# Kernel optimization log

Hardware: AMD Instinct MI355X
Metric: run time of the kernel (lower is better)

The kernel has to match this reference:

```python
import jax, jax.numpy as jnp
import numpy as np

B, CIN, COUT, H, W = 8, 64, 64, 128, 128


def conv2d(x, w, b):
    # NCHW x OIHW -> NCHW, stride 1, SAME padding (kernel 3, pad 1)
    y = jax.lax.conv_general_dilated(
        x, w, window_strides=(1, 1), padding='SAME',
        dimension_numbers=('NCHW', 'OIHW', 'NCHW'))
    return y + b[None, :, None, None]


def bilinear_sample(img, py, px):
    # img: [B, C, H, W]; py, px: [B, K, H, W] float sample coords (y, x)
    # Zero padding outside the image (torchvision DeformConv2d semantics).
    Bn, C, Hn, Wn = img.shape
    y0 = jnp.floor(py)
    x0 = jnp.floor(px)
    wy = py - y0  # [B, K, H, W]
    wx = px - x0
    flat = img.reshape(Bn, C, Hn * Wn)

    def corner(yi, xi):
        valid = (yi >= 0) & (yi < Hn) & (xi >= 0) & (xi < Wn)
        yc = jnp.clip(yi, 0, Hn - 1).astype(jnp.int32)
        xc = jnp.clip(xi, 0, Wn - 1).astype(jnp.int32)
        idx = (yc * Wn + xc).reshape(Bn, -1)  # [B, K*H*W]
        g = jax.vmap(lambda f, i: f[:, i])(flat, idx)  # [B, C, K*H*W]
        g = g.reshape(Bn, C, *py.shape[1:])  # [B, C, K, H, W]
        return g * valid[:, None].astype(img.dtype)

    g00 = corner(y0, x0)
    g01 = corner(y0, x0 + 1)
    g10 = corner(y0 + 1, x0)
    g11 = corner(y0 + 1, x0 + 1)
    wy_ = wy[:, None]  # [B, 1, K, H, W]
    wx_ = wx[:, None]
    return (1 - wy_) * ((1 - wx_) * g00 + wx_ * g01) + wy_ * ((1 - wx_) * g10 + wx_ * g11)


def setup_inputs() -> dict:
    key = jax.random.key(0)
    ks = jax.random.split(key, 4)
    x = jax.random.normal(ks[0], (B, CIN, H, W), dtype=jnp.float32)
    # offset conv: in_channels -> 18 (= 2 * 3 * 3), kernel 3, pad 1
    offset_w = jax.random.normal(ks[1], (18, CIN, 3, 3), dtype=jnp.float32) * 0.01
    offset_b = jnp.zeros((18,), dtype=jnp.float32)
    deform_w = jax.random.normal(ks[2], (COUT, CIN, 3, 3), dtype=jnp.float32) * (1.0 / np.sqrt(CIN * 9))
    deform_b = jnp.zeros((COUT,), dtype=jnp.float32)
    return {'x': x, 'offset_w': offset_w, 'offset_b': offset_b,
            'deform_w': deform_w, 'deform_b': deform_b}


def reference(x, offset_w, offset_b, deform_w, deform_b):
    Bn, C, Hn, Wn = x.shape
    # 1) offset conv
    off = conv2d(x, offset_w, offset_b)  # [B, 18, H, W]
    off = off.reshape(Bn, 9, 2, Hn, Wn)  # per kernel position k: (dy, dx)
    dy = off[:, :, 0]  # [B, 9, H, W]
    dx = off[:, :, 1]
    # 2) sampling positions: p0 + p_k + offset (kernel 3x3, pad 1 -> p_k in {-1,0,1})
    k = jnp.arange(9)
    ki = (k // 3 - 1).astype(jnp.float32)[None, :, None, None]
    kj = (k % 3 - 1).astype(jnp.float32)[None, :, None, None]
    py = jnp.arange(Hn, dtype=jnp.float32)[None, None, :, None] + ki + dy
    px = jnp.arange(Wn, dtype=jnp.float32)[None, None, None, :] + kj + dx
    sampled = bilinear_sample(x, py, px)  # [B, C, 9, H, W]
    # 3) conv accumulation over (C, k)
    w = deform_w.reshape(deform_w.shape[0], C, 9)  # [O, C, 9]
    out = jnp.einsum('bckhw,ock->bohw', sampled, w) + deform_b[None, :, None, None]
    return jax.nn.relu(out)
```

## Files before the change

### kernel.cpp

```cpp
#include <hip/hip_runtime.h>
#include <hip/hip_bf16.h>

#define H_ 128
#define W_ 128
#define B_ 8
#define CIN_ 64
#define COUT_ 64

typedef __attribute__((ext_vector_type(8))) short bf16x8;
typedef __attribute__((ext_vector_type(4))) float f32x4;

static __device__ __forceinline__ unsigned short f2bf(float f) {
  union { float f; unsigned int u; } a; a.f = f;
  unsigned int u = a.u;
  return (unsigned short)((u + 0x7fffu + ((u >> 16) & 1u)) >> 16);
}
static __device__ __forceinline__ float bf2f(unsigned short h) {
  union { unsigned int u; float f; } a; a.u = ((unsigned int)h) << 16; return a.f;
}

__global__ __launch_bounds__(256) void prep_w(const float* __restrict__ dw,
    const float* __restrict__ ow, unsigned short* __restrict__ dwt,
    unsigned short* __restrict__ owt) {
  int id = blockIdx.x * 256 + threadIdx.x;
  if (id < 36864) {
    int c = id & 63, o = (id >> 6) & 63, k = id >> 12;
    dwt[id] = f2bf(dw[(o * 64 + c) * 9 + k]);
  } else if (id < 36864 + 18432) {
    int j = id - 36864;
    int c = j & 63, om = (j >> 6) & 31, t = j >> 11;
    owt[j] = f2bf(om < 18 ? ow[(om * 64 + c) * 9 + t] : 0.f);
  }
}


__device__ __forceinline__ void corner8(const float* __restrict__ x,
    const unsigned short* __restrict__ ldsx, int b, int iy, int ix,
    int oy, int ox, int c8, float g[8]) {
  int ly = iy - oy, lx = ix - ox;
  if ((unsigned)ly < 15u && (unsigned)lx < 16u) {
    int pt = (ly << 4) | lx;
    bf16x8 q = *(const bf16x8*)&ldsx[(pt << 6) | ((c8 ^ (pt & 7)) << 3)];
#pragma unroll
    for (int ci = 0; ci < 8; ++ci) g[ci] = bf2f((unsigned short)q[ci]);
  } else if ((unsigned)iy < (unsigned)H_ && (unsigned)ix < (unsigned)W_) {
#pragma unroll
    for (int ci = 0; ci < 8; ++ci)
      g[ci] = x[((b * CIN_ + (c8 << 3) + ci) * H_ + iy) * W_ + ix];
  } else {
#pragma unroll
    for (int ci = 0; ci < 8; ++ci) g[ci] = 0.f;
  }
}

__global__ __launch_bounds__(256) void deform_main(const float* __restrict__ x,
    const unsigned short* __restrict__ owt, const float* __restrict__ ob,
    const unsigned short* __restrict__ dwt, const float* __restrict__ db,
    float* __restrict__ out) {
  __shared__ unsigned short ldsx[240 * 64];
  __shared__ unsigned short ldsS[64 * 64];
  __shared__ float offs_lds[64][18];
  __shared__ int   p_iy[576], p_ix[576];
  __shared__ float p_wy[576], p_wx[576];

  const int tid = threadIdx.x;
  const int blk = blockIdx.x;
  const int b = blk >> 8;
  const int ty = ((blk >> 4) & 15) << 3;
  const int tx = (blk & 15) << 3;
  const int oy = ty - 3, ox = tx - 4;
  const int lane = tid & 63;
  const int wv = tid >> 6;
  const int o_m = (wv << 4) + (lane & 15);
  const int kgrp = lane >> 4;

  for (int i = 0; i < 15; ++i) {
    int it = tid + (i << 8);
    int c = it / 60;
    int r = it - c * 60;
    int lyy = r >> 2;
    int xq = r & 3;
    int gy = oy + lyy;
    int gx0 = ox + (xq << 2);
    float4 v = make_float4(0.f, 0.f, 0.f, 0.f);
    if ((unsigned)gy < (unsigned)H_ && (unsigned)gx0 < (unsigned)W_)
      v = *(const float4*)&x[((b * CIN_ + c) * H_ + gy) * W_ + gx0];
    int c8 = c >> 3, c0 = c & 7;
    const float vv[4] = {v.x, v.y, v.z, v.w};
#pragma unroll
    for (int q = 0; q < 4; ++q) {
      int pt = (lyy << 4) | ((xq << 2) + q);
      ldsx[(pt << 6) | ((c8 ^ (pt & 7)) << 3) | c0] = f2bf(vv[q]);
    }
  }
  __syncthreads();

  {
    f32x4 aoff0 = (f32x4){0.f, 0.f, 0.f, 0.f};
    f32x4 aoff1 = (f32x4){0.f, 0.f, 0.f, 0.f};
    const int pixw = (wv << 4) | (lane & 15);
#pragma unroll
    for (int t = 0; t < 9; ++t) {
      const int ti = t / 3 - 1, tj = t % 3 - 1;
      const int ly = (pixw >> 3) + ti + 3;
      const int lx = (pixw & 7) + tj + 4;
      const int pt = (ly << 4) | lx;
#pragma unroll
      for (int hf = 0; hf < 2; ++hf) {
        const int c8 = (hf << 2) | kgrp;
        bf16x8 bfr = *(const bf16x8*)&ldsx[(pt << 6) | ((c8 ^ (pt & 7)) << 3)];
        bf16x8 a0 = *(const bf16x8*)&owt[(((t << 5) | (lane & 15)) << 6) | (c8 << 3)];
        bf16x8 a1 = *(const bf16x8*)&owt[(((t << 5) | 16 | (lane & 15)) << 6) | (c8 << 3)];
        aoff0 = __builtin_amdgcn_mfma_f32_16x16x32_bf16(a0, bfr, aoff0, 0, 0, 0);
        aoff1 = __builtin_amdgcn_mfma_f32_16x16x32_bf16(a1, bfr, aoff1, 0, 0, 0);
      }
    }
#pragma unroll
    for (int j = 0; j < 4; ++j) {
      int o = (kgrp << 2) + j;
      offs_lds[pixw][o] = aoff0[j] + ob[o];
      int o1 = 16 + o;
      if (o1 < 18) offs_lds[pixw][o1] = aoff1[j] + ob[o1];
    }
  }
  __syncthreads();

  for (int u = tid; u < 576; u += 256) {
    int pix = u & 63, k = u >> 6;
    int yy = ty + (pix >> 3), xx = tx + (pix & 7);
    float dy = offs_lds[pix][2 * k];
    float dx = offs_lds[pix][2 * k + 1];
    float py = (float)(yy + k / 3 - 1) + dy;
    float px = (float)(xx + k % 3 - 1) + dx;
    float fy = floorf(py), fx = floorf(px);
    p_iy[u] = (int)fy; p_ix[u] = (int)fx;
    p_wy[u] = py - fy; p_wx[u] = px - fx;
  }
  __syncthreads();

  f32x4 acc[4];
#pragma unroll
  for (int nt = 0; nt < 4; ++nt) acc[nt] = (f32x4){0.f, 0.f, 0.f, 0.f};

#pragma unroll
  for (int k = 0; k < 9; ++k) {
    bf16x8 af0 = *(const bf16x8*)&dwt[(k << 12) + (o_m << 6) + (kgrp << 3)];
    bf16x8 af1 = *(const bf16x8*)&dwt[(k << 12) + (o_m << 6) + 32 + (kgrp << 3)];

#pragma unroll
    for (int i = 0; i < 2; ++i) {
      int u = tid + (i << 8);
      int pix = u >> 3, c8 = u & 7;
      int pd = (k << 6) | pix;
      int iy = p_iy[pd], ix = p_ix[pd];
      float wy = p_wy[pd], wx = p_wx[pd];
      float w00 = (1.f - wy) * (1.f - wx), w01 = (1.f - wy) * wx;
      float w10 = wy * (1.f - wx),         w11 = wy * wx;
      float g00[8], g01[8], g10[8], g11[8];
      corner8(x, ldsx, b, iy,     ix,     oy, ox, c8, g00);
      corner8(x, ldsx, b, iy,     ix + 1, oy, ox, c8, g01);
      corner8(x, ldsx, b, iy + 1, ix,     oy, ox, c8, g10);
      corner8(x, ldsx, b, iy + 1, ix + 1, oy, ox, c8, g11);
      bf16x8 sv;
#pragma unroll
      for (int ci = 0; ci < 8; ++ci) {
        float v = g00[ci] * w00 + g01[ci] * w01 + g10[ci] * w10 + g11[ci] * w11;
        sv[ci] = (short)f2bf(v);
      }
      *(bf16x8*)&ldsS[(pix << 6) | ((c8 ^ (pix & 7)) << 3)] = sv;
    }
    __syncthreads();

#pragma unroll
    for (int hf = 0; hf < 2; ++hf) {
#pragma unroll
      for (int nt = 0; nt < 4; ++nt) {
        int pix = (nt << 4) | (lane & 15);
        int c8 = (hf << 2) | kgrp;
        bf16x8 bf = *(const bf16x8*)&ldsS[(pix << 6) | ((c8 ^ (pix & 7)) << 3)];
        acc[nt] = __builtin_amdgcn_mfma_f32_16x16x32_bf16(hf ? af1 : af0, bf, acc[nt], 0, 0, 0);
      }
    }
    __syncthreads();
  }

#pragma unroll
  for (int nt = 0; nt < 4; ++nt) {
    int pix = (nt << 4) | (lane & 15);
    int gy = ty + (pix >> 3), gx = tx + (pix & 7);
#pragma unroll
    for (int j = 0; j < 4; ++j) {
      int o = (wv << 4) + (kgrp << 2) + j;
      float v = acc[nt][j] + db[o];
      out[((b * COUT_ + o) * H_ + gy) * W_ + gx] = v > 0.f ? v : 0.f;
    }
  }
}

extern "C" void kernel_launch(void* const* d_in, const int* in_sizes, int n_in,
                              void* d_out, int out_size, void* d_ws, size_t ws_size,
                              hipStream_t stream) {
  const float* x  = (const float*)d_in[0];
  const float* ow = (const float*)d_in[1];
  const float* ob = (const float*)d_in[2];
  const float* dw = (const float*)d_in[3];
  const float* db = (const float*)d_in[4];
  float* out = (float*)d_out;

  unsigned short* dwt = (unsigned short*)d_ws;
  unsigned short* owt = (unsigned short*)((char*)d_ws + 73728);

  hipLaunchKernelGGL(prep_w, dim3(216), dim3(256), 0, stream, dw, ow, dwt, owt);
  hipLaunchKernelGGL(deform_main, dim3(2048), dim3(256), 0, stream,
                     x, owt, ob, dwt, db, out);
}
```

Baseline: 190.3 us.

## Feed bilinear samples directly into MFMA registers, removing LDS staging and barriers

Each wave now computes bilinear samples for its own 16 pixels straight into the MFMA B-fragment registers. It swaps the roles of the operands so each wave covers all 64 output channels, which removes the ldsS staging buffer, the precomputed sample-position arrays and two barriers per kernel tap. The input tile load is rewritten so that each thread loads one pixel across all channels and packs it with v_cvt_pk_bf16. Launch bounds now request 4 blocks per CU. The cost is that each wave loads more weight fragments from global memory, and the strided per-channel global loads during tile fill coalesce less well.

```diff
diff --git a/kernel.cpp b/kernel.cpp
--- a/kernel.cpp
+++ b/kernel.cpp
@@ -9,14 +9,27 @@
 
 typedef __attribute__((ext_vector_type(8))) short bf16x8;
 typedef __attribute__((ext_vector_type(4))) float f32x4;
+typedef __attribute__((ext_vector_type(4))) unsigned int u32x4;
 
 static __device__ __forceinline__ unsigned short f2bf(float f) {
   union { float f; unsigned int u; } a; a.f = f;
   unsigned int u = a.u;
   return (unsigned short)((u + 0x7fffu + ((u >> 16) & 1u)) >> 16);
 }
-static __device__ __forceinline__ float bf2f(unsigned short h) {
-  union { unsigned int u; float f; } a; a.u = ((unsigned int)h) << 16; return a.f;
+
+static __device__ __forceinline__ unsigned int cvt_pk_bf16(float lo, float hi) {
+  unsigned int r;
+  asm("v_cvt_pk_bf16_f32 %0, %1, %2" : "=v"(r) : "v"(lo), "v"(hi));
+  return r;
+}
+
+static __device__ __forceinline__ void unpack8(const bf16x8& q, float g[8]) {
+  union { bf16x8 v; unsigned int w[4]; } u; u.v = q;
+#pragma unroll
+  for (int j = 0; j < 4; ++j) {
+    g[2 * j]     = __uint_as_float(u.w[j] << 16);
+    g[2 * j + 1] = __uint_as_float(u.w[j] & 0xffff0000u);
+  }
 }
 
 __global__ __launch_bounds__(256) void prep_w(const float* __restrict__ dw,
@@ -41,8 +54,7 @@
   if ((unsigned)ly < 15u && (unsigned)lx < 16u) {
     int pt = (ly << 4) | lx;
     bf16x8 q = *(const bf16x8*)&ldsx[(pt << 6) | ((c8 ^ (pt & 7)) << 3)];
-#pragma unroll
-    for (int ci = 0; ci < 8; ++ci) g[ci] = bf2f((unsigned short)q[ci]);
+    unpack8(q, g);
   } else if ((unsigned)iy < (unsigned)H_ && (unsigned)ix < (unsigned)W_) {
 #pragma unroll
     for (int ci = 0; ci < 8; ++ci)
@@ -53,15 +65,12 @@
   }
 }
 
-__global__ __launch_bounds__(256) void deform_main(const float* __restrict__ x,
+__global__ __launch_bounds__(256, 4) void deform_main(const float* __restrict__ x,
     const unsigned short* __restrict__ owt, const float* __restrict__ ob,
     const unsigned short* __restrict__ dwt, const float* __restrict__ db,
     float* __restrict__ out) {
   __shared__ unsigned short ldsx[240 * 64];
-  __shared__ unsigned short ldsS[64 * 64];
   __shared__ float offs_lds[64][18];
-  __shared__ int   p_iy[576], p_ix[576];
-  __shared__ float p_wy[576], p_wx[576];
 
   const int tid = threadIdx.x;
   const int blk = blockIdx.x;
@@ -71,26 +80,28 @@
   const int oy = ty - 3, ox = tx - 4;
   const int lane = tid & 63;
   const int wv = tid >> 6;
-  const int o_m = (wv << 4) + (lane & 15);
+  const int pl = lane & 15;
   const int kgrp = lane >> 4;
-
-  for (int i = 0; i < 15; ++i) {
-    int it = tid + (i << 8);
-    int c = it / 60;
-    int r = it - c * 60;
-    int lyy = r >> 2;
-    int xq = r & 3;
-    int gy = oy + lyy;
-    int gx0 = ox + (xq << 2);
-    float4 v = make_float4(0.f, 0.f, 0.f, 0.f);
-    if ((unsigned)gy < (unsigned)H_ && (unsigned)gx0 < (unsigned)W_)
-      v = *(const float4*)&x[((b * CIN_ + c) * H_ + gy) * W_ + gx0];
-    int c8 = c >> 3, c0 = c & 7;
-    const float vv[4] = {v.x, v.y, v.z, v.w};
-#pragma unroll
-    for (int q = 0; q < 4; ++q) {
-      int pt = (lyy << 4) | ((xq << 2) + q);
-      ldsx[(pt << 6) | ((c8 ^ (pt & 7)) << 3) | c0] = f2bf(vv[q]);
+  const int pwl = (wv << 4) | pl;
+  const int pyy = ty + (pwl >> 3), pxx = tx + (pwl & 7);
+
+  {
+    int pt = tid;
+    if (pt < 240) {
+      int gy = oy + (pt >> 4), gx = ox + (pt & 15);
+      bool ok = ((unsigned)gy < (unsigned)H_) && ((unsigned)gx < (unsigned)W_);
+      int base = ((b * CIN_) * H_ + gy) * W_ + gx;
+#pragma unroll
+      for (int c8 = 0; c8 < 8; ++c8) {
+        float v[8];
+#pragma unroll
+        for (int ci = 0; ci < 8; ++ci)
+          v[ci] = ok ? x[base + ((c8 << 3) + ci) * (H_ * W_)] : 0.f;
+        u32x4 sv;
+#pragma unroll
+        for (int j = 0; j < 4; ++j) sv[j] = cvt_pk_bf16(v[2 * j], v[2 * j + 1]);
+        *(u32x4*)&ldsx[(pt << 6) | ((c8 ^ (pt & 7)) << 3)] = sv;
+      }
     }
   }
   __syncthreads();
@@ -98,19 +109,17 @@
   {
     f32x4 aoff0 = (f32x4){0.f, 0.f, 0.f, 0.f};
     f32x4 aoff1 = (f32x4){0.f, 0.f, 0.f, 0.f};
-    const int pixw = (wv << 4) | (lane & 15);
 #pragma unroll
     for (int t = 0; t < 9; ++t) {
-      const int ti = t / 3 - 1, tj = t % 3 - 1;
-      const int ly = (pixw >> 3) + ti + 3;
-      const int lx = (pixw & 7) + tj + 4;
+      const int ly = (pwl >> 3) + (t / 3) - 1 + 3;
+      const int lx = (pwl & 7) + (t % 3) - 1 + 4;
       const int pt = (ly << 4) | lx;
 #pragma unroll
       for (int hf = 0; hf < 2; ++hf) {
         const int c8 = (hf << 2) | kgrp;
         bf16x8 bfr = *(const bf16x8*)&ldsx[(pt << 6) | ((c8 ^ (pt & 7)) << 3)];
-        bf16x8 a0 = *(const bf16x8*)&owt[(((t << 5) | (lane & 15)) << 6) | (c8 << 3)];
-        bf16x8 a1 = *(const bf16x8*)&owt[(((t << 5) | 16 | (lane & 15)) << 6) | (c8 << 3)];
+        bf16x8 a0 = *(const bf16x8*)&owt[(((t << 5) | pl) << 6) | (c8 << 3)];
+        bf16x8 a1 = *(const bf16x8*)&owt[(((t << 5) | 16 | pl) << 6) | (c8 << 3)];
         aoff0 = __builtin_amdgcn_mfma_f32_16x16x32_bf16(a0, bfr, aoff0, 0, 0, 0);
         aoff1 = __builtin_amdgcn_mfma_f32_16x16x32_bf16(a1, bfr, aoff1, 0, 0, 0);
       }
@@ -118,81 +127,62 @@
 #pragma unroll
     for (int j = 0; j < 4; ++j) {
       int o = (kgrp << 2) + j;
-      offs_lds[pixw][o] = aoff0[j] + ob[o];
+      offs_lds[pwl][o] = aoff0[j] + ob[o];
       int o1 = 16 + o;
-      if (o1 < 18) offs_lds[pixw][o1] = aoff1[j] + ob[o1];
+      if (o1 < 18) offs_lds[pwl][o1] = aoff1[j] + ob[o1];
     }
   }
   __syncthreads();
 
-  for (int u = tid; u < 576; u += 256) {
-    int pix = u & 63, k = u >> 6;
-    int yy = ty + (pix >> 3), xx = tx + (pix & 7);
-    float dy = offs_lds[pix][2 * k];
-    float dx = offs_lds[pix][2 * k + 1];
-    float py = (float)(yy + k / 3 - 1) + dy;
-    float px = (float)(xx + k % 3 - 1) + dx;
+  f32x4 acc[4];
+#pragma unroll
+  for (int mt = 0; mt < 4; ++mt) acc[mt] = (f32x4){0.f, 0.f, 0.f, 0.f};
+
+#pragma unroll
+  for (int k = 0; k < 9; ++k) {
+    float dy = offs_lds[pwl][2 * k];
+    float dx = offs_lds[pwl][2 * k + 1];
+    float py = (float)(pyy + (k / 3) - 1) + dy;
+    float px = (float)(pxx + (k % 3) - 1) + dx;
     float fy = floorf(py), fx = floorf(px);
-    p_iy[u] = (int)fy; p_ix[u] = (int)fx;
-    p_wy[u] = py - fy; p_wx[u] = px - fx;
-  }
-  __syncthreads();
-
-  f32x4 acc[4];
-#pragma unroll
-  for (int nt = 0; nt < 4; ++nt) acc[nt] = (f32x4){0.f, 0.f, 0.f, 0.f};
-
-#pragma unroll
-  for (int k = 0; k < 9; ++k) {
-    bf16x8 af0 = *(const bf16x8*)&dwt[(k << 12) + (o_m << 6) + (kgrp << 3)];
-    bf16x8 af1 = *(const bf16x8*)&dwt[(k << 12) + (o_m << 6) + 32 + (kgrp << 3)];
-
-#pragma unroll
-    for (int i = 0; i < 2; ++i) {
-      int u = tid + (i << 8);
-      int pix = u >> 3, c8 = u & 7;
-      int pd = (k << 6) | pix;
-      int iy = p_iy[pd], ix = p_ix[pd];
-      float wy = p_wy[pd], wx = p_wx[pd];
-      float w00 = (1.f - wy) * (1.f - wx), w01 = (1.f - wy) * wx;
-      float w10 = wy * (1.f - wx),         w11 = wy * wx;
+    int iy = (int)fy, ix = (int)fx;
+    float wy = py - fy, wx = px - fx;
+    float wy1 = 1.f - wy, wx1 = 1.f - wx;
+    float w00 = wy1 * wx1, w01 = wy1 * wx, w10 = wy * wx1, w11 = wy * wx;
+
+#pragma unroll
+    for (int hf = 0; hf < 2; ++hf) {
+      const int c8 = (hf << 2) | kgrp;
       float g00[8], g01[8], g10[8], g11[8];
       corner8(x, ldsx, b, iy,     ix,     oy, ox, c8, g00);
       corner8(x, ldsx, b, iy,     ix + 1, oy, ox, c8, g01);
       corner8(x, ldsx, b, iy + 1, ix,     oy, ox, c8, g10);
       corner8(x, ldsx, b, iy + 1, ix + 1, oy, ox, c8, g11);
-      bf16x8 sv;
-#pragma unroll
-      for (int ci = 0; ci < 8; ++ci) {
-        float v = g00[ci] * w00 + g01[ci] * w01 + g10[ci] * w10 + g11[ci] * w11;
-        sv[ci] = (short)f2bf(v);
-      }
-      *(bf16x8*)&ldsS[(pix << 6) | ((c8 ^ (pix & 7)) << 3)] = sv;
-    }
-    __syncthreads();
-
-#pragma unroll
-    for (int hf = 0; hf < 2; ++hf) {
-#pragma unroll
-      for (int nt = 0; nt < 4; ++nt) {
-        int pix = (nt << 4) | (lane & 15);
-        int c8 = (hf << 2) | kgrp;
-        bf16x8 bf = *(const bf16x8*)&ldsS[(pix << 6) | ((c8 ^ (pix & 7)) << 3)];
-        acc[nt] = __builtin_amdgcn_mfma_f32_16x16x32_bf16(hf ? af1 : af0, bf, acc[nt], 0, 0, 0);
-      }
-    }
-    __syncthreads();
-  }
-
-#pragma unroll
-  for (int nt = 0; nt < 4; ++nt) {
-    int pix = (nt << 4) | (lane & 15);
-    int gy = ty + (pix >> 3), gx = tx + (pix & 7);
+      union { bf16x8 v; u32x4 w; } bfrag;
+#pragma unroll
+      for (int j = 0; j < 4; ++j) {
+        float v0 = fmaf(g11[2 * j], w11, fmaf(g10[2 * j], w10,
+                   fmaf(g01[2 * j], w01, g00[2 * j] * w00)));
+        float v1 = fmaf(g11[2 * j + 1], w11, fmaf(g10[2 * j + 1], w10,
+                   fmaf(g01[2 * j + 1], w01, g00[2 * j + 1] * w00)));
+        bfrag.w[j] = cvt_pk_bf16(v0, v1);
+      }
+#pragma unroll
+      for (int mt = 0; mt < 4; ++mt) {
+        bf16x8 af = *(const bf16x8*)&dwt[(k << 12) + (((mt << 4) | pl) << 6)
+                                         + (hf << 5) + (kgrp << 3)];
+        acc[mt] = __builtin_amdgcn_mfma_f32_16x16x32_bf16(af, bfrag.v, acc[mt], 0, 0, 0);
+      }
+    }
+  }
+
+#pragma unroll
+  for (int mt = 0; mt < 4; ++mt) {
 #pragma unroll
     for (int j = 0; j < 4; ++j) {
-      int o = (wv << 4) + (kgrp << 2) + j;
-      float v = acc[nt][j] + db[o];
-      out[((b * COUT_ + o) * H_ + gy) * W_ + gx] = v > 0.f ? v : 0.f;
+      int o = (mt << 4) | (kgrp << 2) | j;
+      float v = acc[mt][j] + db[o];
+      out[((b * COUT_ + o) * H_ + pyy) * W_ + pxx] = v > 0.f ? v : 0.f;
     }
   }
 }
```

New measurement: 208.6 us. +9.6%, slower.
